# Optimization experiments

Hardware: AMD Instinct MI355X
Metric: run time of the kernel (lower is better)

## Reference

```python
import jax, jax.numpy as jnp
import numpy as np

TOP_K = 2
EPS = float(np.finfo(np.float64).eps)  # combine() clamps zeros to np.finfo(float).eps


def setup_inputs() -> dict:
    key = jax.random.key(0)
    ks = jax.random.split(key, 6)
    B, D, H, O, E = 2048, 1024, 2048, 512, 8
    return {
        "x": jax.random.normal(ks[0], (B, D), dtype=jnp.float32),
        "w_gate": jax.random.normal(ks[1], (D, E), dtype=jnp.float32) * 0.02,
        "fc1_w": jax.random.normal(ks[2], (E, D, H), dtype=jnp.float32) * 0.02,
        "fc1_b": jax.random.normal(ks[3], (E, H), dtype=jnp.float32) * 0.02,
        "fc2_w": jax.random.normal(ks[4], (E, H, O), dtype=jnp.float32) * 0.02,
        "fc2_b": jax.random.normal(ks[5], (E, O), dtype=jnp.float32) * 0.02,
    }


def _gates(x, w_gate):
    # Noisy top-k gating in eval mode (no noise): clean logits -> top-k -> softmax over top-k -> scatter.
    logits = x @ w_gate                              # [B, E]
    top_logits, top_idx = jax.lax.top_k(logits, TOP_K)  # [B, K]
    top_gates = jax.nn.softmax(top_logits, axis=-1)      # 'softmax' gating over selected experts
    B = x.shape[0]
    gates = jnp.zeros(logits.shape, logits.dtype)
    gates = gates.at[jnp.arange(B)[:, None], top_idx].set(top_gates)
    return gates                                      # [B, E], zero for non-selected experts


def reference(x, w_gate, fc1_w, fc1_b, fc2_w, fc2_b):
    gates = _gates(x, w_gate)                         # [B, E]
    # Dense-equivalent of SparseDispatcher: non-selected experts have gate 0,
    # so weighting by gates reproduces dispatch/expert/combine exactly.
    h = jax.nn.gelu(jnp.einsum('bd,edh->ebh', x, fc1_w) + fc1_b[:, None, :],
                    approximate=False)                # [E, B, H]
    logp = jax.nn.log_softmax(jnp.einsum('ebh,eho->ebo', h, fc2_w) + fc2_b[:, None, :],
                              axis=-1)                # [E, B, O] (MLP ends with LogSoftmax)
    # combine: sum_e gates[b,e] * exp(logp_e[b]), clamp zeros to eps, then log
    combined = jnp.einsum('ebo,be->bo', jnp.exp(logp), gates)  # [B, O]
    combined = jnp.where(combined == 0, jnp.asarray(EPS, combined.dtype), combined)
    return jnp.log(combined)
```

## Files before the change

kernel.cpp:

```cpp
#include <hip/hip_runtime.h>
#include <stdint.h>

#define Bn 2048
#define Dn 1024
#define Hn 2048
#define On 512
#define En 8

typedef float f32x4 __attribute__((ext_vector_type(4)));
typedef unsigned char u8;

__device__ __forceinline__ void gload16(const void* g, void* l) {
  __builtin_amdgcn_global_load_lds((const uint32_t*)g, (uint32_t*)l, 16, 0, 0);
}

__device__ __forceinline__ u8 f2fp8(float v) {
  int w = __builtin_amdgcn_cvt_pk_fp8_f32(v, v, 0, false);
  return (u8)(w & 0xff);
}

__device__ __forceinline__ uint32_t pk4_fp8(float a, float b, float c, float d) {
  int w = __builtin_amdgcn_cvt_pk_fp8_f32(a, b, 0, false);
  w = __builtin_amdgcn_cvt_pk_fp8_f32(c, d, w, true);
  return (uint32_t)w;
}

__global__ void init_kernel(int* counts, int* cursors) {
  int t = threadIdx.x;
  if (t < En) { counts[t] = 0; cursors[t] = 0; }
}

#define NB_G (Bn / 8)
#define NB_T1 ((Dn / 256) * (Hn / 64) * En)
#define NB_T2 ((Hn / 256) * (On / 64) * En)
#define WSCALE 64.0f

__device__ __forceinline__ void tcast_f8_256(const float* __restrict__ inp,
                                             u8* __restrict__ outp,
                                             int R, int C, int r0, int c0, uint32_t* L) {
  int t = threadIdx.x;
  int cc4 = (t & 15) * 4;
  int rg = t >> 4;
#pragma unroll
  for (int p = 0; p < 4; p++) {
    int rbase = p * 64 + rg * 4;
    float4 v0 = *(const float4*)&inp[(size_t)(r0 + rbase + 0) * C + c0 + cc4];
    float4 v1 = *(const float4*)&inp[(size_t)(r0 + rbase + 1) * C + c0 + cc4];
    float4 v2 = *(const float4*)&inp[(size_t)(r0 + rbase + 2) * C + c0 + cc4];
    float4 v3 = *(const float4*)&inp[(size_t)(r0 + rbase + 3) * C + c0 + cc4];
    uint32_t wds[4];
    wds[0] = pk4_fp8(v0.x * WSCALE, v1.x * WSCALE, v2.x * WSCALE, v3.x * WSCALE);
    wds[1] = pk4_fp8(v0.y * WSCALE, v1.y * WSCALE, v2.y * WSCALE, v3.y * WSCALE);
    wds[2] = pk4_fp8(v0.z * WSCALE, v1.z * WSCALE, v2.z * WSCALE, v3.z * WSCALE);
    wds[3] = pk4_fp8(v0.w * WSCALE, v1.w * WSCALE, v2.w * WSCALE, v3.w * WSCALE);
    int rd = p * 16 + rg;
#pragma unroll
    for (int j = 0; j < 4; j++) L[(cc4 + j) * 65 + rd] = wds[j];
  }
  __syncthreads();
  int c = t >> 2, q = t & 3;
  uint32_t dw[16];
#pragma unroll
  for (int i = 0; i < 16; i++) dw[i] = L[c * 65 + q * 16 + i];
  u8* op = &outp[(size_t)(c0 + c) * R + r0 + q * 64];
#pragma unroll
  for (int s = 0; s < 4; s++) {
    int4 o = make_int4((int)dw[4 * s], (int)dw[4 * s + 1], (int)dw[4 * s + 2],
                       (int)dw[4 * s + 3]);
    *(int4*)(op + 16 * s) = o;
  }
}

__global__ __launch_bounds__(256) void prep_kernel(
    const float* __restrict__ x, const float* __restrict__ wg,
    const float* __restrict__ fc1w, const float* __restrict__ fc2w,
    u8* __restrict__ x_f8, u8* __restrict__ w1t8, u8* __restrict__ w2t8,
    int* __restrict__ top_idx, float* __restrict__ gates, int* __restrict__ counts) {
  __shared__ __align__(16) uint32_t smem[64 * 65];
  __shared__ int lcnt[En];
  int bid = blockIdx.x;
  int t = threadIdx.x;

  if (bid < NB_G) {
    if (t < En) lcnt[t] = 0;
    __syncthreads();
    int w = t >> 6, lane = t & 63;
#pragma unroll
    for (int r = 0; r < 2; r++) {
      int b = bid * 8 + w * 2 + r;
      const float4* xr = (const float4*)(x + (size_t)b * Dn) + lane * 4;
      float acc[En];
#pragma unroll
      for (int e = 0; e < En; e++) acc[e] = 0.f;
      uint32_t xw[4];
#pragma unroll
      for (int q = 0; q < 4; q++) {
        float4 v = xr[q];
        xw[q] = pk4_fp8(v.x, v.y, v.z, v.w);
        int d0 = lane * 16 + q * 4;
        const float* wp = wg + (size_t)d0 * En;
#pragma unroll
        for (int i = 0; i < 4; i++) {
          float xv = ((const float*)&v)[i];
          float4 wa = *(const float4*)(wp + i * En);
          float4 wb = *(const float4*)(wp + i * En + 4);
          acc[0] += xv * wa.x; acc[1] += xv * wa.y;
          acc[2] += xv * wa.z; acc[3] += xv * wa.w;
          acc[4] += xv * wb.x; acc[5] += xv * wb.y;
          acc[6] += xv * wb.z; acc[7] += xv * wb.w;
        }
      }
      *(int4*)(x_f8 + (size_t)b * Dn + lane * 16) =
          make_int4((int)xw[0], (int)xw[1], (int)xw[2], (int)xw[3]);
#pragma unroll
      for (int off = 32; off; off >>= 1) {
#pragma unroll
        for (int e = 0; e < En; e++) acc[e] += __shfl_down(acc[e], off);
      }
      if (lane == 0) {
        float best = -1e30f, second = -1e30f; int bi = 0, si = 0;
#pragma unroll
        for (int e = 0; e < En; e++) {
          float l = acc[e];
          if (l > best) { second = best; si = bi; best = l; bi = e; }
          else if (l > second) { second = l; si = e; }
        }
        float e1 = expf(second - best);
        float inv = 1.f / (1.f + e1);
        top_idx[2 * b] = bi; top_idx[2 * b + 1] = si;
        gates[2 * b] = inv;  gates[2 * b + 1] = e1 * inv;
        atomicAdd(&lcnt[bi], 1);
        atomicAdd(&lcnt[si], 1);
      }
    }
    __syncthreads();
    if (t < En) {
      int c = lcnt[t];
      if (c) atomicAdd(&counts[t], c);
    }
  } else if (bid < NB_G + NB_T1) {
    int idx = bid - NB_G;
    constexpr int TPE = (Dn / 256) * (Hn / 64);
    int z = idx / TPE, rem = idx % TPE;
    int r0 = (rem / (Hn / 64)) * 256, c0 = (rem % (Hn / 64)) * 64;
    tcast_f8_256(fc1w + (size_t)z * Dn * Hn, w1t8 + (size_t)z * Dn * Hn, Dn, Hn, r0, c0, smem);
  } else {
    int idx = bid - NB_G - NB_T1;
    constexpr int TPE = (Hn / 256) * (On / 64);
    int z = idx / TPE, rem = idx % TPE;
    int r0 = (rem / (On / 64)) * 256, c0 = (rem % (On / 64)) * 64;
    tcast_f8_256(fc2w + (size_t)z * Hn * On, w2t8 + (size_t)z * Hn * On, Hn, On, r0, c0, smem);
  }
}

__global__ void assign_kernel(const int* __restrict__ top_idx, const int* __restrict__ counts,
                              int* cursors, int* __restrict__ s2r, int* __restrict__ r2s) {
  int b = blockIdx.x * 256 + threadIdx.x;
  if (b >= Bn) return;
  int offs[En];
  int s = 0;
#pragma unroll
  for (int e = 0; e < En; e++) { offs[e] = s; s += counts[e]; }
#pragma unroll
  for (int k = 0; k < 2; k++) {
    int e = top_idx[2 * b + k];
    int pos = atomicAdd(&cursors[e], 1);
    int slot = offs[e] + pos;
    s2r[slot] = b;
    r2s[2 * b + k] = slot;
  }
}

template <bool FC1, int N, int K, int SPLITK>
__global__ __launch_bounds__(256, 8) void fp8_gemm_kernel(
    const u8* __restrict__ A, const u8* __restrict__ WT,
    const float* __restrict__ bias, const int* __restrict__ counts,
    const int* __restrict__ s2r,
    u8* __restrict__ outH8, float* __restrict__ outL, float* __restrict__ outLX) {
  constexpr int NBL = N / 64;
  constexpr int KS = K / SPLITK;
  constexpr int NT = KS / 64;
  int e = blockIdx.z;
  int cnt = counts[e];
  int rb = blockIdx.y;
  if (rb * 64 >= cnt) return;
  int base = 0;
#pragma unroll
  for (int i = 0; i < En; i++) base += (i < e) ? counts[i] : 0;
  int ks = blockIdx.x / NBL;
  int nb = (blockIdx.x % NBL) * 64;
  int k0 = ks * KS;
  __shared__ __align__(16) u8 As[64 * 64];
  __shared__ __align__(16) u8 Bs[64 * 64];
  int t = threadIdx.x;
  int lane = t & 63, w = t >> 6;
  int wr = w >> 1, wc = w & 1;

  int srow = t >> 2;
  int sslot = (t & 3) ^ ((srow >> 1) & 3);
  int scol = sslot * 16;

  int lr = rb * 64 + srow;
  int lrc = lr < cnt ? lr : cnt - 1;
  const u8* aptr = A + (size_t)(FC1 ? s2r[base + lrc] : (base + lrc)) * K + k0 + scol;
  const u8* bptr = WT + ((size_t)e * N + nb + srow) * K + k0 + scol;

  f32x4 zero = {0.f, 0.f, 0.f, 0.f};
  f32x4 acc[2][2];
#pragma unroll
  for (int m = 0; m < 2; m++)
#pragma unroll
    for (int n = 0; n < 2; n++) acc[m][n] = zero;

  int a_r = wr * 32 + (lane & 15);
  int b_r = wc * 32 + (lane & 15);
  int rkey = ((lane & 15) >> 1) & 3;
  int slb = (lane >> 4) >> 1;
  int half = ((lane >> 4) & 1) * 8;

  for (int kt = 0; kt < NT; kt++) {
    gload16(aptr + kt * 64, &As[t * 16]);
    gload16(bptr + kt * 64, &Bs[t * 16]);
    __syncthreads();
#pragma unroll
    for (int kk = 0; kk < 2; kk++) {
      long af[2], bfr[2];
#pragma unroll
      for (int m = 0; m < 2; m++)
        af[m] = *(const long*)(As + (a_r + m * 16) * 64 +
                               (((kk * 2 + slb) ^ rkey) << 4) + half);
#pragma unroll
      for (int n = 0; n < 2; n++)
        bfr[n] = *(const long*)(Bs + (b_r + n * 16) * 64 +
                                (((kk * 2 + slb) ^ rkey) << 4) + half);
#pragma unroll
      for (int m = 0; m < 2; m++)
#pragma unroll
        for (int n = 0; n < 2; n++)
          acc[m][n] = __builtin_amdgcn_mfma_f32_16x16x32_fp8_fp8(af[m], bfr[n], acc[m][n], 0, 0, 0);
    }
    __syncthreads();
  }

  const float INV = 1.0f / WSCALE;
  float* dst = (SPLITK > 1 && ks > 0) ? (outLX + (size_t)(ks - 1) * (2 * Bn * On)) : outL;
  int lr0 = rb * 64 + wr * 32;
#pragma unroll
  for (int m = 0; m < 2; m++) {
#pragma unroll
    for (int i = 0; i < 4; i++) {
      int orow = lr0 + m * 16 + (lane >> 4) * 4 + i;
      if (orow < cnt) {
        int slot = base + orow;
#pragma unroll
        for (int n = 0; n < 2; n++) {
          int col = nb + wc * 32 + n * 16 + (lane & 15);
          if (FC1) {
            float v = acc[m][n][i] * INV + bias[e * N + col];
            float g = 0.5f * v * (1.0f + erff(v * 0.70710678118654752f));
            outH8[(size_t)slot * N + col] = f2fp8(g);
          } else {
            float v = acc[m][n][i] * INV + (ks == 0 ? bias[e * N + col] : 0.f);
            dst[(size_t)slot * N + col] = v;
          }
        }
      }
    }
  }
}

__device__ __forceinline__ float blk_reduce(float v, bool ismax) {
  __shared__ float sbuf[4];
  int lane = threadIdx.x & 63, w = threadIdx.x >> 6;
#pragma unroll
  for (int off = 32; off; off >>= 1) {
    float o = __shfl_down(v, off);
    v = ismax ? fmaxf(v, o) : (v + o);
  }
  __syncthreads();
  if (lane == 0) sbuf[w] = v;
  __syncthreads();
  float r = sbuf[0];
#pragma unroll
  for (int i = 1; i < 4; i++) r = ismax ? fmaxf(r, sbuf[i]) : (r + sbuf[i]);
  return r;
}

__global__ void combine_kernel(const float* __restrict__ l2a, const float* __restrict__ l2x,
                               const int* __restrict__ r2s, const float* __restrict__ gates,
                               float* __restrict__ out) {
  int b = blockIdx.x, t = threadIdx.x;
  float c0 = 0.f, c1 = 0.f;
#pragma unroll
  for (int k = 0; k < 2; k++) {
    int slot = r2s[2 * b + k];
    float g = gates[2 * b + k];
    const float* lp0 = l2a + (size_t)slot * On;
    const float* lp1 = l2x + (size_t)slot * On;
    float v0 = lp0[t] + lp1[t];
    float v1 = lp0[t + 256] + lp1[t + 256];
    float m = blk_reduce(fmaxf(v0, v1), true);
    float s = blk_reduce(expf(v0 - m) + expf(v1 - m), false);
    float lse = m + logf(s);
    c0 += g * expf(v0 - lse);
    c1 += g * expf(v1 - lse);
  }
  const float EPSv = 2.220446049250313e-16f;
  out[(size_t)b * On + t] = logf(fmaxf(c0, EPSv));
  out[(size_t)b * On + t + 256] = logf(fmaxf(c1, EPSv));
}

extern "C" void kernel_launch(void* const* d_in, const int* in_sizes, int n_in,
                              void* d_out, int out_size, void* d_ws, size_t ws_size,
                              hipStream_t stream) {
  const float* x = (const float*)d_in[0];
  const float* wgate = (const float*)d_in[1];
  const float* fc1w = (const float*)d_in[2];
  const float* fc1b = (const float*)d_in[3];
  const float* fc2w = (const float*)d_in[4];
  const float* fc2b = (const float*)d_in[5];
  float* out = (float*)d_out;

  char* ws = (char*)d_ws;
  size_t o = 0;
  u8* x_f8      = (u8*)(ws + o);    o += (size_t)Bn * Dn;
  u8* w1t8      = (u8*)(ws + o);    o += (size_t)En * Hn * Dn;
  u8* w2t8      = (u8*)(ws + o);    o += (size_t)En * On * Hn;
  u8* hbuf8     = (u8*)(ws + o);    o += (size_t)2 * Bn * Hn;
  float* l2buf  = (float*)(ws + o); o += (size_t)2 * Bn * On * 4;
  float* l2bufX = (float*)(ws + o); o += (size_t)2 * Bn * On * 4;
  int* top_idx  = (int*)(ws + o);   o += (size_t)Bn * 2 * 4;
  float* gates  = (float*)(ws + o); o += (size_t)Bn * 2 * 4;
  int* r2s      = (int*)(ws + o);   o += (size_t)Bn * 2 * 4;
  int* s2r      = (int*)(ws + o);   o += (size_t)2 * Bn * 4;
  int* counts   = (int*)(ws + o);   o += 64;
  int* cursors  = (int*)(ws + o);   o += 64;

  hipLaunchKernelGGL(init_kernel, dim3(1), dim3(64), 0, stream, counts, cursors);
  hipLaunchKernelGGL(prep_kernel, dim3(NB_G + NB_T1 + NB_T2), dim3(256), 0, stream,
                     x, wgate, fc1w, fc2w, x_f8, w1t8, w2t8, top_idx, gates, counts);
  hipLaunchKernelGGL(assign_kernel, dim3(Bn / 256), dim3(256), 0, stream,
                     top_idx, counts, cursors, s2r, r2s);
  hipLaunchKernelGGL((fp8_gemm_kernel<true, Hn, Dn, 1>), dim3(Hn / 64, 32, En), dim3(256),
                     0, stream, x_f8, w1t8, fc1b, counts, s2r, hbuf8,
                     (float*)nullptr, (float*)nullptr);
  hipLaunchKernelGGL((fp8_gemm_kernel<false, On, Hn, 2>), dim3((On / 64) * 2, 32, En), dim3(256),
                     0, stream, hbuf8, w2t8, fc2b, counts, s2r, (u8*)nullptr,
                     l2buf, l2bufX);
  hipLaunchKernelGGL(combine_kernel, dim3(Bn), dim3(256), 0, stream, l2buf, l2bufX, r2s, gates, out);
}
```

Before: 117.5 us.

## Move fc2 weight transpose-cast into fc1 GEMM launch and simplify gate loads

Takes the fc2 weight FP8 transpose-cast out of the prep kernel and runs it as extra tail blocks of the fc1 GEMM launch, using a smaller 64x64 tile routine. The aim is to shorten the prep kernel's critical path and let the weight conversion fill idle CUs, since many fc1 blocks exit early because of sparse routing. The gating pass now reads x with a lane-strided scalar pattern and writes FP8 bytes one at a time instead of using float4 loads and packed stores. That may coalesce better but issues more, smaller memory operations. The fc1 GEMM is split into its own kernel with a 1D grid.

```diff
diff --git a/kernel.cpp b/kernel.cpp
--- a/kernel.cpp
+++ b/kernel.cpp
@@ -30,10 +30,9 @@
   if (t < En) { counts[t] = 0; cursors[t] = 0; }
 }
 
+#define WSCALE 64.0f
 #define NB_G (Bn / 8)
 #define NB_T1 ((Dn / 256) * (Hn / 64) * En)
-#define NB_T2 ((Hn / 256) * (On / 64) * En)
-#define WSCALE 64.0f
 
 __device__ __forceinline__ void tcast_f8_256(const float* __restrict__ inp,
                                              u8* __restrict__ outp,
@@ -71,10 +70,35 @@
   }
 }
 
+__device__ __forceinline__ void tcast_f8_64(const float* __restrict__ inp,
+                                            u8* __restrict__ outp,
+                                            int R, int C, int r0, int c0, uint32_t* L) {
+  int t = threadIdx.x;
+  int cc4 = (t & 15) * 4;
+  int rg = t >> 4;
+  float4 v0 = *(const float4*)&inp[(size_t)(r0 + rg * 4 + 0) * C + c0 + cc4];
+  float4 v1 = *(const float4*)&inp[(size_t)(r0 + rg * 4 + 1) * C + c0 + cc4];
+  float4 v2 = *(const float4*)&inp[(size_t)(r0 + rg * 4 + 2) * C + c0 + cc4];
+  float4 v3 = *(const float4*)&inp[(size_t)(r0 + rg * 4 + 3) * C + c0 + cc4];
+  uint32_t wds[4];
+  wds[0] = pk4_fp8(v0.x * WSCALE, v1.x * WSCALE, v2.x * WSCALE, v3.x * WSCALE);
+  wds[1] = pk4_fp8(v0.y * WSCALE, v1.y * WSCALE, v2.y * WSCALE, v3.y * WSCALE);
+  wds[2] = pk4_fp8(v0.z * WSCALE, v1.z * WSCALE, v2.z * WSCALE, v3.z * WSCALE);
+  wds[3] = pk4_fp8(v0.w * WSCALE, v1.w * WSCALE, v2.w * WSCALE, v3.w * WSCALE);
+#pragma unroll
+  for (int j = 0; j < 4; j++) L[(cc4 + j) * 17 + rg] = wds[j];
+  __syncthreads();
+  int c = t >> 2, q = t & 3;
+  int4 o;
+#pragma unroll
+  for (int i = 0; i < 4; i++) ((int*)&o)[i] = (int)L[c * 17 + q * 4 + i];
+  *(int4*)&outp[(size_t)(c0 + c) * R + r0 + q * 16] = o;
+}
+
 __global__ __launch_bounds__(256) void prep_kernel(
     const float* __restrict__ x, const float* __restrict__ wg,
-    const float* __restrict__ fc1w, const float* __restrict__ fc2w,
-    u8* __restrict__ x_f8, u8* __restrict__ w1t8, u8* __restrict__ w2t8,
+    const float* __restrict__ fc1w,
+    u8* __restrict__ x_f8, u8* __restrict__ w1t8,
     int* __restrict__ top_idx, float* __restrict__ gates, int* __restrict__ counts) {
   __shared__ __align__(16) uint32_t smem[64 * 65];
   __shared__ int lcnt[En];
@@ -88,30 +112,23 @@
 #pragma unroll
     for (int r = 0; r < 2; r++) {
       int b = bid * 8 + w * 2 + r;
-      const float4* xr = (const float4*)(x + (size_t)b * Dn) + lane * 4;
+      const float* xr = x + (size_t)b * Dn;
+      u8* xo = x_f8 + (size_t)b * Dn;
       float acc[En];
 #pragma unroll
       for (int e = 0; e < En; e++) acc[e] = 0.f;
-      uint32_t xw[4];
-#pragma unroll
-      for (int q = 0; q < 4; q++) {
-        float4 v = xr[q];
-        xw[q] = pk4_fp8(v.x, v.y, v.z, v.w);
-        int d0 = lane * 16 + q * 4;
-        const float* wp = wg + (size_t)d0 * En;
-#pragma unroll
-        for (int i = 0; i < 4; i++) {
-          float xv = ((const float*)&v)[i];
-          float4 wa = *(const float4*)(wp + i * En);
-          float4 wb = *(const float4*)(wp + i * En + 4);
-          acc[0] += xv * wa.x; acc[1] += xv * wa.y;
-          acc[2] += xv * wa.z; acc[3] += xv * wa.w;
-          acc[4] += xv * wb.x; acc[5] += xv * wb.y;
-          acc[6] += xv * wb.z; acc[7] += xv * wb.w;
-        }
+#pragma unroll
+      for (int j = 0; j < 16; j++) {
+        int d = lane + j * 64;
+        float xv = xr[d];
+        xo[d] = f2fp8(xv);
+        float4 wa = *(const float4*)(wg + (size_t)d * En);
+        float4 wb = *(const float4*)(wg + (size_t)d * En + 4);
+        acc[0] += xv * wa.x; acc[1] += xv * wa.y;
+        acc[2] += xv * wa.z; acc[3] += xv * wa.w;
+        acc[4] += xv * wb.x; acc[5] += xv * wb.y;
+        acc[6] += xv * wb.z; acc[7] += xv * wb.w;
       }
-      *(int4*)(x_f8 + (size_t)b * Dn + lane * 16) =
-          make_int4((int)xw[0], (int)xw[1], (int)xw[2], (int)xw[3]);
 #pragma unroll
       for (int off = 32; off; off >>= 1) {
 #pragma unroll
@@ -138,18 +155,12 @@
       int c = lcnt[t];
       if (c) atomicAdd(&counts[t], c);
     }
-  } else if (bid < NB_G + NB_T1) {
+  } else {
     int idx = bid - NB_G;
     constexpr int TPE = (Dn / 256) * (Hn / 64);
     int z = idx / TPE, rem = idx % TPE;
     int r0 = (rem / (Hn / 64)) * 256, c0 = (rem % (Hn / 64)) * 64;
     tcast_f8_256(fc1w + (size_t)z * Dn * Hn, w1t8 + (size_t)z * Dn * Hn, Dn, Hn, r0, c0, smem);
-  } else {
-    int idx = bid - NB_G - NB_T1;
-    constexpr int TPE = (Hn / 256) * (On / 64);
-    int z = idx / TPE, rem = idx % TPE;
-    int r0 = (rem / (On / 64)) * 256, c0 = (rem % (On / 64)) * 64;
-    tcast_f8_256(fc2w + (size_t)z * Hn * On, w2t8 + (size_t)z * Hn * On, Hn, On, r0, c0, smem);
   }
 }
 
@@ -171,12 +182,110 @@
   }
 }
 
-template <bool FC1, int N, int K, int SPLITK>
-__global__ __launch_bounds__(256, 8) void fp8_gemm_kernel(
+__global__ __launch_bounds__(256, 8) void fc1_fused_kernel(
     const u8* __restrict__ A, const u8* __restrict__ WT,
     const float* __restrict__ bias, const int* __restrict__ counts,
-    const int* __restrict__ s2r,
-    u8* __restrict__ outH8, float* __restrict__ outL, float* __restrict__ outLX) {
+    const int* __restrict__ s2r, u8* __restrict__ outH8,
+    const float* __restrict__ fc2w, u8* __restrict__ w2t8) {
+  __shared__ __align__(16) u8 shbuf[8192];
+  int bid = blockIdx.x;
+  int t = threadIdx.x;
+  if (bid >= 8192) {
+    int idx = bid - 8192;
+    constexpr int TPE = (Hn / 64) * (On / 64);
+    int z = idx / TPE, rem = idx % TPE;
+    int r0 = (rem / (On / 64)) * 64, c0 = (rem % (On / 64)) * 64;
+    tcast_f8_64(fc2w + (size_t)z * Hn * On, w2t8 + (size_t)z * Hn * On, Hn, On, r0, c0,
+                (uint32_t*)shbuf);
+    return;
+  }
+  constexpr int K = Dn, N = Hn;
+  constexpr int NT = K / 64;
+  int e = bid >> 10;
+  int rb = (bid >> 5) & 31;
+  int nb = (bid & 31) * 64;
+  int cnt = counts[e];
+  if (rb * 64 >= cnt) return;
+  int base = 0;
+#pragma unroll
+  for (int i = 0; i < En; i++) base += (i < e) ? counts[i] : 0;
+  u8* As = shbuf;
+  u8* Bs = shbuf + 4096;
+  int lane = t & 63, w = t >> 6;
+  int wr = w >> 1, wc = w & 1;
+
+  int srow = t >> 2;
+  int sslot = (t & 3) ^ ((srow >> 1) & 3);
+  int scol = sslot * 16;
+
+  int lr = rb * 64 + srow;
+  int lrc = lr < cnt ? lr : cnt - 1;
+  const u8* aptr = A + (size_t)s2r[base + lrc] * K + scol;
+  const u8* bptr = WT + ((size_t)e * N + nb + srow) * K + scol;
+
+  f32x4 zero = {0.f, 0.f, 0.f, 0.f};
+  f32x4 acc[2][2];
+#pragma unroll
+  for (int m = 0; m < 2; m++)
+#pragma unroll
+    for (int n = 0; n < 2; n++) acc[m][n] = zero;
+
+  int a_r = wr * 32 + (lane & 15);
+  int b_r = wc * 32 + (lane & 15);
+  int rkey = ((lane & 15) >> 1) & 3;
+  int slb = (lane >> 4) >> 1;
+  int half = ((lane >> 4) & 1) * 8;
+
+  for (int kt = 0; kt < NT; kt++) {
+    gload16(aptr + kt * 64, &As[t * 16]);
+    gload16(bptr + kt * 64, &Bs[t * 16]);
+    __syncthreads();
+#pragma unroll
+    for (int kk = 0; kk < 2; kk++) {
+      long af[2], bfr[2];
+#pragma unroll
+      for (int m = 0; m < 2; m++)
+        af[m] = *(const long*)(As + (a_r + m * 16) * 64 +
+                               (((kk * 2 + slb) ^ rkey) << 4) + half);
+#pragma unroll
+      for (int n = 0; n < 2; n++)
+        bfr[n] = *(const long*)(Bs + (b_r + n * 16) * 64 +
+                                (((kk * 2 + slb) ^ rkey) << 4) + half);
+#pragma unroll
+      for (int m = 0; m < 2; m++)
+#pragma unroll
+        for (int n = 0; n < 2; n++)
+          acc[m][n] = __builtin_amdgcn_mfma_f32_16x16x32_fp8_fp8(af[m], bfr[n], acc[m][n], 0, 0, 0);
+    }
+    __syncthreads();
+  }
+
+  const float INV = 1.0f / WSCALE;
+  int lr0 = rb * 64 + wr * 32;
+#pragma unroll
+  for (int m = 0; m < 2; m++) {
+#pragma unroll
+    for (int i = 0; i < 4; i++) {
+      int orow = lr0 + m * 16 + (lane >> 4) * 4 + i;
+      if (orow < cnt) {
+        int slot = base + orow;
+#pragma unroll
+        for (int n = 0; n < 2; n++) {
+          int col = nb + wc * 32 + n * 16 + (lane & 15);
+          float v = acc[m][n][i] * INV + bias[e * N + col];
+          float g = 0.5f * v * (1.0f + erff(v * 0.70710678118654752f));
+          outH8[(size_t)slot * N + col] = f2fp8(g);
+        }
+      }
+    }
+  }
+}
+
+template <int N, int K, int SPLITK>
+__global__ __launch_bounds__(256, 8) void fc2_gemm_kernel(
+    const u8* __restrict__ A, const u8* __restrict__ WT,
+    const float* __restrict__ bias, const int* __restrict__ counts,
+    float* __restrict__ outL, float* __restrict__ outLX) {
   constexpr int NBL = N / 64;
   constexpr int KS = K / SPLITK;
   constexpr int NT = KS / 64;
@@ -202,7 +311,7 @@
 
   int lr = rb * 64 + srow;
   int lrc = lr < cnt ? lr : cnt - 1;
-  const u8* aptr = A + (size_t)(FC1 ? s2r[base + lrc] : (base + lrc)) * K + k0 + scol;
+  const u8* aptr = A + (size_t)(base + lrc) * K + k0 + scol;
   const u8* bptr = WT + ((size_t)e * N + nb + srow) * K + k0 + scol;
 
   f32x4 zero = {0.f, 0.f, 0.f, 0.f};
@@ -243,7 +352,7 @@
   }
 
   const float INV = 1.0f / WSCALE;
-  float* dst = (SPLITK > 1 && ks > 0) ? (outLX + (size_t)(ks - 1) * (2 * Bn * On)) : outL;
+  float* dst = (ks > 0) ? outLX : outL;
   int lr0 = rb * 64 + wr * 32;
 #pragma unroll
   for (int m = 0; m < 2; m++) {
@@ -255,14 +364,8 @@
 #pragma unroll
         for (int n = 0; n < 2; n++) {
           int col = nb + wc * 32 + n * 16 + (lane & 15);
-          if (FC1) {
-            float v = acc[m][n][i] * INV + bias[e * N + col];
-            float g = 0.5f * v * (1.0f + erff(v * 0.70710678118654752f));
-            outH8[(size_t)slot * N + col] = f2fp8(g);
-          } else {
-            float v = acc[m][n][i] * INV + (ks == 0 ? bias[e * N + col] : 0.f);
-            dst[(size_t)slot * N + col] = v;
-          }
+          float v = acc[m][n][i] * INV + (ks == 0 ? bias[e * N + col] : 0.f);
+          dst[(size_t)slot * N + col] = v;
         }
       }
     }
@@ -337,15 +440,13 @@
   int* cursors  = (int*)(ws + o);   o += 64;
 
   hipLaunchKernelGGL(init_kernel, dim3(1), dim3(64), 0, stream, counts, cursors);
-  hipLaunchKernelGGL(prep_kernel, dim3(NB_G + NB_T1 + NB_T2), dim3(256), 0, stream,
-                     x, wgate, fc1w, fc2w, x_f8, w1t8, w2t8, top_idx, gates, counts);
+  hipLaunchKernelGGL(prep_kernel, dim3(NB_G + NB_T1), dim3(256), 0, stream,
+                     x, wgate, fc1w, x_f8, w1t8, top_idx, gates, counts);
   hipLaunchKernelGGL(assign_kernel, dim3(Bn / 256), dim3(256), 0, stream,
                      top_idx, counts, cursors, s2r, r2s);
-  hipLaunchKernelGGL((fp8_gemm_kernel<true, Hn, Dn, 1>), dim3(Hn / 64, 32, En), dim3(256),
-                     0, stream, x_f8, w1t8, fc1b, counts, s2r, hbuf8,
-                     (float*)nullptr, (float*)nullptr);
-  hipLaunchKernelGGL((fp8_gemm_kernel<false, On, Hn, 2>), dim3((On / 64) * 2, 32, En), dim3(256),
-                     0, stream, hbuf8, w2t8, fc2b, counts, s2r, (u8*)nullptr,
-                     l2buf, l2bufX);
+  hipLaunchKernelGGL(fc1_fused_kernel, dim3(8192 + 2048), dim3(256), 0, stream,
+                     x_f8, w1t8, fc1b, counts, s2r, hbuf8, fc2w, w2t8);
+  hipLaunchKernelGGL((fc2_gemm_kernel<On, Hn, 2>), dim3((On / 64) * 2, 32, En), dim3(256),
+                     0, stream, hbuf8, w2t8, fc2b, counts, l2buf, l2bufX);
   hipLaunchKernelGGL(combine_kernel, dim3(Bn), dim3(256), 0, stream, l2buf, l2bufX, r2s, gates, out);
 }
```

New measurement: 115.3 us. Within noise of the previous version (-1.9%).
